# Performance work log

Hardware: AMD Instinct MI355X
Metric: run time of the kernel (lower is better)

Reference implementation:

```python
import jax, jax.numpy as jnp
import numpy as np

BSZ, T, D_IN, P, H, D_OUT = 8, 4096, 512, 256, 256, 512


def setup_inputs() -> dict:
    key = jax.random.key(0)
    ks = jax.random.split(key, 8)
    x_seq = jax.random.normal(ks[0], (BSZ, T, D_IN), dtype=jnp.float32)
    # stable diagonal transition: |a| < 1 so the 4096-step recurrence does not blow up
    a = jax.random.uniform(ks[1], (H,), minval=-0.99, maxval=0.99, dtype=jnp.float32)
    B = jax.random.normal(ks[2], (P, H), dtype=jnp.float32) * 0.05
    C = jax.random.normal(ks[3], (H, P), dtype=jnp.float32) * 0.05
    Wi = jax.random.normal(ks[4], (P, D_IN), dtype=jnp.float32) * 0.05
    bi = jax.random.normal(ks[5], (P,), dtype=jnp.float32) * 0.05
    Wo = jax.random.normal(ks[6], (D_OUT, P), dtype=jnp.float32) * 0.05
    bo = jax.random.normal(ks[7], (D_OUT,), dtype=jnp.float32) * 0.05
    return {"x_seq": x_seq, "a": a, "B": B, "C": C, "Wi": Wi, "bi": bi, "Wo": Wo, "bo": bo}


def reference(x_seq, a, B, C, Wi, bi, Wo, bo):
    # proj_in + relu (eqx.nn.Linear: y = W @ x + b), vmapped over batch and time
    x_proj = jax.nn.relu(jnp.einsum("btd,pd->btp", x_seq, Wi) + bi)  # [Bsz,T,P]
    # precompute driving input u_t = B^T x_t for every step
    u = jnp.einsum("btp,ph->bth", x_proj, B)  # [Bsz,T,H]
    u_t = jnp.swapaxes(u, 0, 1)  # [T,Bsz,H] (scan over time)

    def step(h, u_step):  # h: [Bsz,H]
        h = a * h + u_step
        return h, h

    h0 = jnp.zeros((x_seq.shape[0], a.shape[0]), dtype=x_seq.dtype)
    _, hs = jax.lax.scan(step, h0, u_t)  # hs: [T,Bsz,H]
    # y_t = C^T h_t, then proj_out
    y_seq = jnp.einsum("tbh,hp->btp", hs, C)  # [Bsz,T,P]
    y_out = jnp.einsum("btp,op->bto", y_seq, Wo) + bo  # [Bsz,T,D_out]
    return y_out
```

## Files before the change

kernel.cpp:

```cpp
#include <hip/hip_runtime.h>

#define BSZN 8
#define TT 4096
#define DIN 512
#define PP 256
#define HHH 256
#define DOUT 512
#define LCH 32
#define NCH (TT / LCH)
#define NBLK (BSZN * NCH)
#define XPS 264

typedef __attribute__((ext_vector_type(8))) short bf16x8;
typedef __attribute__((ext_vector_type(4))) float f32x4;

static __device__ __forceinline__ unsigned short f2bf(float x) {
  union { float f; unsigned u; } t{x};
  unsigned r = t.u + 0x7fffu + ((t.u >> 16) & 1u);
  return (unsigned short)(r >> 16);
}


__global__ __launch_bounds__(256) void prep_k(
    const float* __restrict__ Wi, const float* __restrict__ Wo,
    const float* __restrict__ Cm, const float* __restrict__ Bm,
    unsigned short* __restrict__ Wi_t, unsigned short* __restrict__ B_t,
    unsigned short* __restrict__ C_t, unsigned short* __restrict__ Wo_t) {
  const int b = blockIdx.x, tid = threadIdx.x;
  if (b < 128) {
    const int idx = b * 1024 + tid * 4;
    const int row = idx >> 9, d = idx & 511;
    const float4 v = *(const float4*)(Wi + idx);
    uint2 w;
    w.x = (unsigned)f2bf(v.x) | ((unsigned)f2bf(v.y) << 16);
    w.y = (unsigned)f2bf(v.z) | ((unsigned)f2bf(v.w) << 16);
    const int tile = d >> 5, kc = (d >> 3) & 3, s = (kc + (row >> 1)) & 3;
    *(uint2*)(Wi_t + tile * 8192 + row * 32 + s * 8 + (d & 7)) = w;
  } else if (b < 192) {
    const int f = (b - 128) * 256 + tid;
    const int p = f >> 6, h = (f & 63) * 4;
    const float4 v = *(const float4*)(Bm + (size_t)p * HHH + h);
    const float vv[4] = {v.x, v.y, v.z, v.w};
    const int tile = p >> 5, kc = (p >> 3) & 3;
#pragma unroll
    for (int j = 0; j < 4; ++j) {
      const int row = h + j, s = (kc + (row >> 1)) & 3;
      B_t[tile * 8192 + row * 32 + s * 8 + (p & 7)] = f2bf(vv[j]);
    }
  } else if (b < 256) {
    const int f = (b - 192) * 256 + tid;
    const int h = f >> 6, p = (f & 63) * 4;
    const float4 v = *(const float4*)(Cm + (size_t)h * PP + p);
    const float vv[4] = {v.x, v.y, v.z, v.w};
    const int tile = h >> 5, kc = (h >> 3) & 3;
#pragma unroll
    for (int j = 0; j < 4; ++j) {
      const int row = p + j, s = (kc + (row >> 1)) & 3;
      C_t[tile * 8192 + row * 32 + s * 8 + (h & 7)] = f2bf(vv[j]);
    }
  } else {
    const int idx = (b - 256) * 1024 + tid * 4;
    const int o = idx >> 8, p = idx & 255;
    const float4 v = *(const float4*)(Wo + idx);
    uint2 w;
    w.x = (unsigned)f2bf(v.x) | ((unsigned)f2bf(v.y) << 16);
    w.y = (unsigned)f2bf(v.z) | ((unsigned)f2bf(v.w) << 16);
    const int tile = p >> 5, kc = (p >> 3) & 3, s = (kc + (o >> 1)) & 3;
    *(uint2*)(Wo_t + tile * 16384 + o * 32 + s * 8 + (p & 7)) = w;
  }
}

__global__ __launch_bounds__(256, 4) void s4_scan(
    const float* __restrict__ x, const float* __restrict__ a,
    const unsigned short* __restrict__ Wi_t, const float* __restrict__ bi,
    const unsigned short* __restrict__ B_t, unsigned int* __restrict__ hs0_g,
    float* __restrict__ carry_g) {
  __shared__ alignas(16) char smem[16896];
  unsigned short* xs = (unsigned short*)smem;
  unsigned short* xp = (unsigned short*)smem;

  const int tid = threadIdx.x, wave = tid >> 6, lane = tid & 63;
  const int l15 = lane & 15, q = lane >> 4;
  const int bc = blockIdx.x;
  const size_t row0 = (size_t)bc * LCH;
  const int wc = wave * 64;

  int wrot[4];
#pragma unroll
  for (int ni = 0; ni < 4; ++ni) {
    const int r = wc + ni * 16 + l15;
    wrot[ni] = r * 64 + (((q + (r >> 1)) & 3) << 4);
  }
  int xpb[2];
#pragma unroll
  for (int mi = 0; mi < 2; ++mi) xpb[mi] = (mi * 16 + l15) * XPS + q * 8;

  f32x4 acc[2][4];
#pragma unroll
  for (int i = 0; i < 2; ++i)
#pragma unroll
    for (int j = 0; j < 4; ++j) acc[i][j] = f32x4{0.f, 0.f, 0.f, 0.f};

  for (int hh = 0; hh < 2; ++hh) {
    {
      float4 xv[8];
#pragma unroll
      for (int i = 0; i < 8; ++i) {
        const int f = i * 256 + tid;
        xv[i] = *(const float4*)(x + (row0 + (f >> 6)) * DIN + hh * 256 +
                                 (f & 63) * 4);
      }
#pragma unroll
      for (int i = 0; i < 8; ++i) {
        const int f = i * 256 + tid;
        uint2 w;
        w.x = (unsigned)f2bf(xv[i].x) | ((unsigned)f2bf(xv[i].y) << 16);
        w.y = (unsigned)f2bf(xv[i].z) | ((unsigned)f2bf(xv[i].w) << 16);
        *(uint2*)(xs + (f >> 6) * XPS + (f & 63) * 4) = w;
      }
    }
    __syncthreads();
    const char* WiB = (const char*)Wi_t + hh * 8 * 16384;
    for (int t = 0; t < 4; ++t) {
      bf16x8 af[2][2], bfv[4][2];
#pragma unroll
      for (int mi = 0; mi < 2; ++mi) {
        af[mi][0] = *(const bf16x8*)(xs + xpb[mi] + t * 64);
        af[mi][1] = *(const bf16x8*)(xs + xpb[mi] + t * 64 + 32);
      }
#pragma unroll
      for (int ni = 0; ni < 4; ++ni) {
        bfv[ni][0] = *(const bf16x8*)(WiB + (t * 2) * 16384 + wrot[ni]);
        bfv[ni][1] = *(const bf16x8*)(WiB + (t * 2 + 1) * 16384 + wrot[ni]);
      }
#pragma unroll
      for (int kk = 0; kk < 2; ++kk)
#pragma unroll
        for (int mi = 0; mi < 2; ++mi)
#pragma unroll
          for (int ni = 0; ni < 4; ++ni)
            acc[mi][ni] = __builtin_amdgcn_mfma_f32_16x16x32_bf16(
                af[mi][kk], bfv[ni][kk], acc[mi][ni], 0, 0, 0);
    }
    __syncthreads();
  }

#pragma unroll
  for (int ni = 0; ni < 4; ++ni) {
    const int col = wc + ni * 16 + l15;
    const float bb = bi[col];
#pragma unroll
    for (int mi = 0; mi < 2; ++mi)
#pragma unroll
      for (int reg = 0; reg < 4; ++reg) {
        const int row = mi * 16 + q * 4 + reg;
        xp[row * XPS + col] = f2bf(fmaxf(acc[mi][ni][reg] + bb, 0.f));
      }
  }
  __syncthreads();

#pragma unroll
  for (int i = 0; i < 2; ++i)
#pragma unroll
    for (int j = 0; j < 4; ++j) acc[i][j] = f32x4{0.f, 0.f, 0.f, 0.f};
  {
    const char* BB = (const char*)B_t;
    for (int t = 0; t < 4; ++t) {
      bf16x8 af[2][2], bfv[4][2];
#pragma unroll
      for (int mi = 0; mi < 2; ++mi) {
        af[mi][0] = *(const bf16x8*)(xp + xpb[mi] + t * 64);
        af[mi][1] = *(const bf16x8*)(xp + xpb[mi] + t * 64 + 32);
      }
#pragma unroll
      for (int ni = 0; ni < 4; ++ni) {
        bfv[ni][0] = *(const bf16x8*)(BB + (t * 2) * 16384 + wrot[ni]);
        bfv[ni][1] = *(const bf16x8*)(BB + (t * 2 + 1) * 16384 + wrot[ni]);
      }
#pragma unroll
      for (int kk = 0; kk < 2; ++kk)
#pragma unroll
        for (int mi = 0; mi < 2; ++mi)
#pragma unroll
          for (int ni = 0; ni < 4; ++ni)
            acc[mi][ni] = __builtin_amdgcn_mfma_f32_16x16x32_bf16(
                af[mi][kk], bfv[ni][kk], acc[mi][ni], 0, 0, 0);
    }
  }

  float aC[4], Wz[4];
#pragma unroll
  for (int ni = 0; ni < 4; ++ni) aC[ni] = a[wc + ni * 16 + l15];
#pragma unroll
  for (int ni = 0; ni < 4; ++ni) {
    const float A = aC[ni];
    const float A2 = A * A, A4 = A2 * A2, A8 = A4 * A4, A16 = A8 * A8;
    const float A4q = ((q & 1) ? A4 : 1.f) * ((q & 2) ? A8 : 1.f);
    float W = 0.f;
#pragma unroll
    for (int mi = 0; mi < 2; ++mi) {
      f32x4 v = acc[mi][ni];
      v.y = fmaf(A, v.x, v.y);
      v.z = fmaf(A, v.y, v.z);
      v.w = fmaf(A, v.z, v.w);
      const float E = v.w;
      const float E0 = __shfl(E, l15, 64);
      const float E1 = __shfl(E, l15 + 16, 64);
      const float E2 = __shfl(E, l15 + 32, 64);
      const float E3 = __shfl(E, l15 + 48, 64);
      const float s1 = E0, s2 = fmaf(A4, s1, E1), s3 = fmaf(A4, s2, E2);
      const float s4 = fmaf(A4, s3, E3);
      const float Sq = (q == 0) ? 0.f : (q == 1) ? s1 : (q == 2) ? s2 : s3;
      const float sin_ = fmaf(A4q, W, Sq);
      v.x = fmaf(A, sin_, v.x);
      v.y = fmaf(A2, sin_, v.y);
      v.z = fmaf(A2 * A, sin_, v.z);
      v.w = fmaf(A4, sin_, v.w);
      acc[mi][ni] = v;
      W = fmaf(A16, W, s4);
    }
    Wz[ni] = W;
  }
  if (q == 0) {
#pragma unroll
    for (int ni = 0; ni < 4; ++ni)
      carry_g[(size_t)bc * HHH + wc + ni * 16 + l15] = Wz[ni];
  }
#pragma unroll
  for (int ni = 0; ni < 4; ++ni)
#pragma unroll
    for (int mi = 0; mi < 2; ++mi) {
      const f32x4 v = acc[mi][ni];
      uint2 pk;
      pk.x = (unsigned)f2bf(v.x) | ((unsigned)f2bf(v.y) << 16);
      pk.y = (unsigned)f2bf(v.z) | ((unsigned)f2bf(v.w) << 16);
      const size_t e =
          (((size_t)bc * 4 + wave) * 8 + ni * 2 + mi) * 64 + lane;
      *(uint2*)(hs0_g + e * 2) = pk;
    }
}

__global__ __launch_bounds__(256) void s4_prefix(
    const float* __restrict__ a, const float* __restrict__ carry_g,
    float* __restrict__ P_g) {
  const int b = blockIdx.x, t = threadIdx.x;
  float A = a[t];
#pragma unroll
  for (int j = 0; j < 5; ++j) A *= A;
  const float* cg = carry_g + (size_t)b * NCH * HHH + t;
  float* pg = P_g + (size_t)b * NCH * HHH + t;
  float P = 0.f;
  for (int c0 = 0; c0 < NCH; c0 += 16) {
    float cv[16];
#pragma unroll
    for (int i = 0; i < 16; ++i) cv[i] = cg[(size_t)(c0 + i) * HHH];
#pragma unroll
    for (int i = 0; i < 16; ++i) {
      pg[(size_t)(c0 + i) * HHH] = P;
      P = fmaf(A, P, cv[i]);
    }
  }
}

__global__ __launch_bounds__(256, 4) void s4_out(
    const float* __restrict__ a, const unsigned int* __restrict__ hs0_g,
    const float* __restrict__ P_g, const unsigned short* __restrict__ C_t,
    const unsigned short* __restrict__ Wo_t, const float* __restrict__ bo,
    float* __restrict__ out) {
  __shared__ alignas(16) char smem[16896];
  unsigned short* hsL = (unsigned short*)smem;

  const int tid = threadIdx.x, wave = tid >> 6, lane = tid & 63;
  const int l15 = lane & 15, q = lane >> 4;
  const int bc = blockIdx.x;
  const size_t row0 = (size_t)bc * LCH;
  const int wc = wave * 64;

  int wrot[4];
#pragma unroll
  for (int ni = 0; ni < 4; ++ni) {
    const int r = wc + ni * 16 + l15;
    wrot[ni] = r * 64 + (((q + (r >> 1)) & 3) << 4);
  }
  int crot[2][4];
#pragma unroll
  for (int g = 0; g < 2; ++g)
#pragma unroll
    for (int ni = 0; ni < 4; ++ni) {
      const int r = wave * 128 + g * 64 + ni * 16 + l15;
      crot[g][ni] = r * 64 + (((q + (r >> 1)) & 3) << 4);
    }
  int xpb[2];
#pragma unroll
  for (int mi = 0; mi < 2; ++mi) xpb[mi] = (mi * 16 + l15) * XPS + q * 8;

  f32x4 acc[2][4];
#pragma unroll
  for (int ni = 0; ni < 4; ++ni)
#pragma unroll
    for (int mi = 0; mi < 2; ++mi) {
      const size_t e =
          (((size_t)bc * 4 + wave) * 8 + ni * 2 + mi) * 64 + lane;
      const uint2 pk = *(const uint2*)(hs0_g + e * 2);
      f32x4 v;
      v.x = __uint_as_float(pk.x << 16);
      v.y = __uint_as_float(pk.x & 0xffff0000u);
      v.z = __uint_as_float(pk.y << 16);
      v.w = __uint_as_float(pk.y & 0xffff0000u);
      acc[mi][ni] = v;
    }
#pragma unroll
  for (int ni = 0; ni < 4; ++ni) {
    const int col = wc + ni * 16 + l15;
    const float A = a[col];
    const float P = P_g[(size_t)bc * HHH + col];
    const float A2 = A * A, A4 = A2 * A2, A8 = A4 * A4, A16 = A8 * A8;
    const float A4q = ((q & 1) ? A4 : 1.f) * ((q & 2) ? A8 : 1.f);
    float fm = A4q * A * P;
#pragma unroll
    for (int mi = 0; mi < 2; ++mi) {
      f32x4 v = acc[mi][ni];
      v.x += fm;
      v.y = fmaf(A, fm, v.y);
      v.z = fmaf(A2, fm, v.z);
      v.w = fmaf(A2 * A, fm, v.w);
      acc[mi][ni] = v;
      fm *= A16;
    }
  }
#pragma unroll
  for (int ni = 0; ni < 4; ++ni) {
    const int col = wc + ni * 16 + l15;
#pragma unroll
    for (int mi = 0; mi < 2; ++mi)
#pragma unroll
      for (int reg = 0; reg < 4; ++reg)
        hsL[(mi * 16 + q * 4 + reg) * XPS + col] = f2bf(acc[mi][ni][reg]);
  }
  __syncthreads();

#pragma unroll
  for (int i = 0; i < 2; ++i)
#pragma unroll
    for (int j = 0; j < 4; ++j) acc[i][j] = f32x4{0.f, 0.f, 0.f, 0.f};
  {
    const char* CB = (const char*)C_t;
    for (int t = 0; t < 4; ++t) {
      bf16x8 af[2][2], bfv[4][2];
#pragma unroll
      for (int mi = 0; mi < 2; ++mi) {
        af[mi][0] = *(const bf16x8*)(hsL + xpb[mi] + t * 64);
        af[mi][1] = *(const bf16x8*)(hsL + xpb[mi] + t * 64 + 32);
      }
#pragma unroll
      for (int ni = 0; ni < 4; ++ni) {
        bfv[ni][0] = *(const bf16x8*)(CB + (t * 2) * 16384 + wrot[ni]);
        bfv[ni][1] = *(const bf16x8*)(CB + (t * 2 + 1) * 16384 + wrot[ni]);
      }
#pragma unroll
      for (int kk = 0; kk < 2; ++kk)
#pragma unroll
        for (int mi = 0; mi < 2; ++mi)
#pragma unroll
          for (int ni = 0; ni < 4; ++ni)
            acc[mi][ni] = __builtin_amdgcn_mfma_f32_16x16x32_bf16(
                af[mi][kk], bfv[ni][kk], acc[mi][ni], 0, 0, 0);
    }
  }
  __syncthreads();

#pragma unroll
  for (int ni = 0; ni < 4; ++ni) {
    const int col = wc + ni * 16 + l15;
#pragma unroll
    for (int mi = 0; mi < 2; ++mi)
#pragma unroll
      for (int reg = 0; reg < 4; ++reg)
        hsL[(mi * 16 + q * 4 + reg) * XPS + col] = f2bf(acc[mi][ni][reg]);
  }
  __syncthreads();

  const char* WoB = (const char*)Wo_t;
#pragma unroll
  for (int g = 0; g < 2; ++g) {
    f32x4 oacc[2][4];
#pragma unroll
    for (int i = 0; i < 2; ++i)
#pragma unroll
      for (int j = 0; j < 4; ++j) oacc[i][j] = f32x4{0.f, 0.f, 0.f, 0.f};
    for (int t = 0; t < 8; ++t) {
      bf16x8 af[2], bfv[4];
#pragma unroll
      for (int mi = 0; mi < 2; ++mi)
        af[mi] = *(const bf16x8*)(hsL + xpb[mi] + t * 32);
#pragma unroll
      for (int ni = 0; ni < 4; ++ni)
        bfv[ni] = *(const bf16x8*)(WoB + t * 32768 + crot[g][ni]);
#pragma unroll
      for (int mi = 0; mi < 2; ++mi)
#pragma unroll
        for (int ni = 0; ni < 4; ++ni)
          oacc[mi][ni] = __builtin_amdgcn_mfma_f32_16x16x32_bf16(
              af[mi], bfv[ni], oacc[mi][ni], 0, 0, 0);
    }
#pragma unroll
    for (int ni = 0; ni < 4; ++ni) {
      const int ocol = wave * 128 + g * 64 + ni * 16 + l15;
      const float bb = bo[ocol];
#pragma unroll
      for (int mi = 0; mi < 2; ++mi)
#pragma unroll
        for (int reg = 0; reg < 4; ++reg) {
          const int row = mi * 16 + q * 4 + reg;
          out[(row0 + row) * DOUT + ocol] = oacc[mi][ni][reg] + bb;
        }
    }
  }
}

extern "C" void kernel_launch(void* const* d_in, const int* in_sizes, int n_in,
                              void* d_out, int out_size, void* d_ws,
                              size_t ws_size, hipStream_t stream) {
  const float* x  = (const float*)d_in[0];
  const float* a  = (const float*)d_in[1];
  const float* Bm = (const float*)d_in[2];
  const float* Cm = (const float*)d_in[3];
  const float* Wi = (const float*)d_in[4];
  const float* bi = (const float*)d_in[5];
  const float* Wo = (const float*)d_in[6];
  const float* bo = (const float*)d_in[7];
  float* out = (float*)d_out;

  char* ws = (char*)d_ws;
  unsigned short* Wi_t = (unsigned short*)ws; ws += (size_t)PP * DIN * 2;
  unsigned short* B_t  = (unsigned short*)ws; ws += (size_t)HHH * PP * 2;
  unsigned short* C_t  = (unsigned short*)ws; ws += (size_t)HHH * PP * 2;
  unsigned short* Wo_t = (unsigned short*)ws; ws += (size_t)DOUT * PP * 2;
  float* carry_g = (float*)ws; ws += (size_t)NBLK * HHH * 4;
  float* P_g     = (float*)ws; ws += (size_t)NBLK * HHH * 4;
  unsigned int* hs0_g = (unsigned int*)ws;

  prep_k<<<384, 256, 0, stream>>>(Wi, Wo, Cm, Bm, Wi_t, B_t, C_t, Wo_t);
  s4_scan<<<NBLK, 256, 0, stream>>>(x, a, Wi_t, bi, B_t, hs0_g, carry_g);
  s4_prefix<<<BSZN, 256, 0, stream>>>(a, carry_g, P_g);
  s4_out<<<NBLK, 256, 0, stream>>>(a, hs0_g, P_g, C_t, Wo_t, bo, out);
}
```

Measured before the change: 164.2 us.

## Double-buffer weight fragments in registers and stagger K order per block

Each MFMA k-loop in the scan and output kernels now prefetches the next step's weight fragments into a register double buffer. The k-order is also rotated by block index so blocks read different weight tiles at the same time. The hs0 intermediate and the final output use nontemporal loads and stores, and launch bounds drop from 4 to 2 waves per SIMD so the extra live registers fit. The aim is to hide global and L2 weight-load latency and cut cache pollution from streaming data. The cost is higher register pressure and possibly lower occupancy.

```diff
diff --git a/kernel.cpp b/kernel.cpp
--- a/kernel.cpp
+++ b/kernel.cpp
@@ -70,7 +70,7 @@
   }
 }
 
-__global__ __launch_bounds__(256, 4) void s4_scan(
+__global__ __launch_bounds__(256, 2) void s4_scan(
     const float* __restrict__ x, const float* __restrict__ a,
     const unsigned short* __restrict__ Wi_t, const float* __restrict__ bi,
     const unsigned short* __restrict__ B_t, unsigned int* __restrict__ hs0_g,
@@ -84,6 +84,7 @@
   const int bc = blockIdx.x;
   const size_t row0 = (size_t)bc * LCH;
   const int wc = wave * 64;
+  const int tb = bc & 3;
 
   int wrot[4];
 #pragma unroll
@@ -121,17 +122,32 @@
     }
     __syncthreads();
     const char* WiB = (const char*)Wi_t + hh * 8 * 16384;
-    for (int t = 0; t < 4; ++t) {
-      bf16x8 af[2][2], bfv[4][2];
+    bf16x8 pf[2][4][2];
+    {
+#pragma unroll
+      for (int ni = 0; ni < 4; ++ni) {
+        pf[0][ni][0] = *(const bf16x8*)(WiB + (tb * 2) * 16384 + wrot[ni]);
+        pf[0][ni][1] = *(const bf16x8*)(WiB + (tb * 2 + 1) * 16384 + wrot[ni]);
+      }
+    }
+#pragma unroll
+    for (int tt = 0; tt < 4; ++tt) {
+      const int cur = tt & 1, nxt = cur ^ 1;
+      const int tr = (tt + tb) & 3;
+      if (tt < 3) {
+        const int tn = (tt + 1 + tb) & 3;
+#pragma unroll
+        for (int ni = 0; ni < 4; ++ni) {
+          pf[nxt][ni][0] = *(const bf16x8*)(WiB + (tn * 2) * 16384 + wrot[ni]);
+          pf[nxt][ni][1] =
+              *(const bf16x8*)(WiB + (tn * 2 + 1) * 16384 + wrot[ni]);
+        }
+      }
+      bf16x8 af[2][2];
 #pragma unroll
       for (int mi = 0; mi < 2; ++mi) {
-        af[mi][0] = *(const bf16x8*)(xs + xpb[mi] + t * 64);
-        af[mi][1] = *(const bf16x8*)(xs + xpb[mi] + t * 64 + 32);
-      }
-#pragma unroll
-      for (int ni = 0; ni < 4; ++ni) {
-        bfv[ni][0] = *(const bf16x8*)(WiB + (t * 2) * 16384 + wrot[ni]);
-        bfv[ni][1] = *(const bf16x8*)(WiB + (t * 2 + 1) * 16384 + wrot[ni]);
+        af[mi][0] = *(const bf16x8*)(xs + xpb[mi] + tr * 64);
+        af[mi][1] = *(const bf16x8*)(xs + xpb[mi] + tr * 64 + 32);
       }
 #pragma unroll
       for (int kk = 0; kk < 2; ++kk)
@@ -140,7 +156,7 @@
 #pragma unroll
           for (int ni = 0; ni < 4; ++ni)
             acc[mi][ni] = __builtin_amdgcn_mfma_f32_16x16x32_bf16(
-                af[mi][kk], bfv[ni][kk], acc[mi][ni], 0, 0, 0);
+                af[mi][kk], pf[cur][ni][kk], acc[mi][ni], 0, 0, 0);
     }
     __syncthreads();
   }
@@ -165,17 +181,30 @@
     for (int j = 0; j < 4; ++j) acc[i][j] = f32x4{0.f, 0.f, 0.f, 0.f};
   {
     const char* BB = (const char*)B_t;
-    for (int t = 0; t < 4; ++t) {
-      bf16x8 af[2][2], bfv[4][2];
+    bf16x8 pf[2][4][2];
+#pragma unroll
+    for (int ni = 0; ni < 4; ++ni) {
+      pf[0][ni][0] = *(const bf16x8*)(BB + (tb * 2) * 16384 + wrot[ni]);
+      pf[0][ni][1] = *(const bf16x8*)(BB + (tb * 2 + 1) * 16384 + wrot[ni]);
+    }
+#pragma unroll
+    for (int tt = 0; tt < 4; ++tt) {
+      const int cur = tt & 1, nxt = cur ^ 1;
+      const int tr = (tt + tb) & 3;
+      if (tt < 3) {
+        const int tn = (tt + 1 + tb) & 3;
+#pragma unroll
+        for (int ni = 0; ni < 4; ++ni) {
+          pf[nxt][ni][0] = *(const bf16x8*)(BB + (tn * 2) * 16384 + wrot[ni]);
+          pf[nxt][ni][1] =
+              *(const bf16x8*)(BB + (tn * 2 + 1) * 16384 + wrot[ni]);
+        }
+      }
+      bf16x8 af[2][2];
 #pragma unroll
       for (int mi = 0; mi < 2; ++mi) {
-        af[mi][0] = *(const bf16x8*)(xp + xpb[mi] + t * 64);
-        af[mi][1] = *(const bf16x8*)(xp + xpb[mi] + t * 64 + 32);
-      }
-#pragma unroll
-      for (int ni = 0; ni < 4; ++ni) {
-        bfv[ni][0] = *(const bf16x8*)(BB + (t * 2) * 16384 + wrot[ni]);
-        bfv[ni][1] = *(const bf16x8*)(BB + (t * 2 + 1) * 16384 + wrot[ni]);
+        af[mi][0] = *(const bf16x8*)(xp + xpb[mi] + tr * 64);
+        af[mi][1] = *(const bf16x8*)(xp + xpb[mi] + tr * 64 + 32);
       }
 #pragma unroll
       for (int kk = 0; kk < 2; ++kk)
@@ -184,7 +213,7 @@
 #pragma unroll
           for (int ni = 0; ni < 4; ++ni)
             acc[mi][ni] = __builtin_amdgcn_mfma_f32_16x16x32_bf16(
-                af[mi][kk], bfv[ni][kk], acc[mi][ni], 0, 0, 0);
+                af[mi][kk], pf[cur][ni][kk], acc[mi][ni], 0, 0, 0);
     }
   }
 
@@ -231,12 +260,16 @@
 #pragma unroll
     for (int mi = 0; mi < 2; ++mi) {
       const f32x4 v = acc[mi][ni];
-      uint2 pk;
-      pk.x = (unsigned)f2bf(v.x) | ((unsigned)f2bf(v.y) << 16);
-      pk.y = (unsigned)f2bf(v.z) | ((unsigned)f2bf(v.w) << 16);
+      unsigned long long pk =
+          (unsigned long long)((unsigned)f2bf(v.x) |
+                               ((unsigned)f2bf(v.y) << 16)) |
+          ((unsigned long long)((unsigned)f2bf(v.z) |
+                                ((unsigned)f2bf(v.w) << 16))
+           << 32);
       const size_t e =
           (((size_t)bc * 4 + wave) * 8 + ni * 2 + mi) * 64 + lane;
-      *(uint2*)(hs0_g + e * 2) = pk;
+      __builtin_nontemporal_store(
+          pk, (unsigned long long*)(hs0_g + e * 2));
     }
 }
 
@@ -262,7 +295,7 @@
   }
 }
 
-__global__ __launch_bounds__(256, 4) void s4_out(
+__global__ __launch_bounds__(256, 2) void s4_out(
     const float* __restrict__ a, const unsigned int* __restrict__ hs0_g,
     const float* __restrict__ P_g, const unsigned short* __restrict__ C_t,
     const unsigned short* __restrict__ Wo_t, const float* __restrict__ bo,
@@ -275,6 +308,7 @@
   const int bc = blockIdx.x;
   const size_t row0 = (size_t)bc * LCH;
   const int wc = wave * 64;
+  const int tb = bc & 3, tb8 = bc & 7;
 
   int wrot[4];
 #pragma unroll
@@ -301,12 +335,13 @@
     for (int mi = 0; mi < 2; ++mi) {
       const size_t e =
           (((size_t)bc * 4 + wave) * 8 + ni * 2 + mi) * 64 + lane;
-      const uint2 pk = *(const uint2*)(hs0_g + e * 2);
+      const unsigned long long pk = __builtin_nontemporal_load(
+          (const unsigned long long*)(hs0_g + e * 2));
       f32x4 v;
-      v.x = __uint_as_float(pk.x << 16);
-      v.y = __uint_as_float(pk.x & 0xffff0000u);
-      v.z = __uint_as_float(pk.y << 16);
-      v.w = __uint_as_float(pk.y & 0xffff0000u);
+      v.x = __uint_as_float((unsigned)(pk & 0xffffu) << 16);
+      v.y = __uint_as_float((unsigned)(pk & 0xffff0000u));
+      v.z = __uint_as_float((unsigned)((pk >> 32) & 0xffffu) << 16);
+      v.w = __uint_as_float((unsigned)((pk >> 48) & 0xffffu) << 16);
       acc[mi][ni] = v;
     }
 #pragma unroll
@@ -345,17 +380,30 @@
     for (int j = 0; j < 4; ++j) acc[i][j] = f32x4{0.f, 0.f, 0.f, 0.f};
   {
     const char* CB = (const char*)C_t;
-    for (int t = 0; t < 4; ++t) {
-      bf16x8 af[2][2], bfv[4][2];
+    bf16x8 pf[2][4][2];
+#pragma unroll
+    for (int ni = 0; ni < 4; ++ni) {
+      pf[0][ni][0] = *(const bf16x8*)(CB + (tb * 2) * 16384 + wrot[ni]);
+      pf[0][ni][1] = *(const bf16x8*)(CB + (tb * 2 + 1) * 16384 + wrot[ni]);
+    }
+#pragma unroll
+    for (int tt = 0; tt < 4; ++tt) {
+      const int cur = tt & 1, nxt = cur ^ 1;
+      const int tr = (tt + tb) & 3;
+      if (tt < 3) {
+        const int tn = (tt + 1 + tb) & 3;
+#pragma unroll
+        for (int ni = 0; ni < 4; ++ni) {
+          pf[nxt][ni][0] = *(const bf16x8*)(CB + (tn * 2) * 16384 + wrot[ni]);
+          pf[nxt][ni][1] =
+              *(const bf16x8*)(CB + (tn * 2 + 1) * 16384 + wrot[ni]);
+        }
+      }
+      bf16x8 af[2][2];
 #pragma unroll
       for (int mi = 0; mi < 2; ++mi) {
-        af[mi][0] = *(const bf16x8*)(hsL + xpb[mi] + t * 64);
-        af[mi][1] = *(const bf16x8*)(hsL + xpb[mi] + t * 64 + 32);
-      }
-#pragma unroll
-      for (int ni = 0; ni < 4; ++ni) {
-        bfv[ni][0] = *(const bf16x8*)(CB + (t * 2) * 16384 + wrot[ni]);
-        bfv[ni][1] = *(const bf16x8*)(CB + (t * 2 + 1) * 16384 + wrot[ni]);
+        af[mi][0] = *(const bf16x8*)(hsL + xpb[mi] + tr * 64);
+        af[mi][1] = *(const bf16x8*)(hsL + xpb[mi] + tr * 64 + 32);
       }
 #pragma unroll
       for (int kk = 0; kk < 2; ++kk)
@@ -364,7 +412,7 @@
 #pragma unroll
           for (int ni = 0; ni < 4; ++ni)
             acc[mi][ni] = __builtin_amdgcn_mfma_f32_16x16x32_bf16(
-                af[mi][kk], bfv[ni][kk], acc[mi][ni], 0, 0, 0);
+                af[mi][kk], pf[cur][ni][kk], acc[mi][ni], 0, 0, 0);
     }
   }
   __syncthreads();
@@ -388,20 +436,30 @@
     for (int i = 0; i < 2; ++i)
 #pragma unroll
       for (int j = 0; j < 4; ++j) oacc[i][j] = f32x4{0.f, 0.f, 0.f, 0.f};
-    for (int t = 0; t < 8; ++t) {
-      bf16x8 af[2], bfv[4];
+    bf16x8 pf[2][4];
+#pragma unroll
+    for (int ni = 0; ni < 4; ++ni)
+      pf[0][ni] = *(const bf16x8*)(WoB + tb8 * 32768 + crot[g][ni]);
+#pragma unroll
+    for (int tt = 0; tt < 8; ++tt) {
+      const int cur = tt & 1, nxt = cur ^ 1;
+      const int tr = (tt + tb8) & 7;
+      if (tt < 7) {
+        const int tn = (tt + 1 + tb8) & 7;
+#pragma unroll
+        for (int ni = 0; ni < 4; ++ni)
+          pf[nxt][ni] = *(const bf16x8*)(WoB + tn * 32768 + crot[g][ni]);
+      }
+      bf16x8 af[2];
 #pragma unroll
       for (int mi = 0; mi < 2; ++mi)
-        af[mi] = *(const bf16x8*)(hsL + xpb[mi] + t * 32);
-#pragma unroll
-      for (int ni = 0; ni < 4; ++ni)
-        bfv[ni] = *(const bf16x8*)(WoB + t * 32768 + crot[g][ni]);
+        af[mi] = *(const bf16x8*)(hsL + xpb[mi] + tr * 32);
 #pragma unroll
       for (int mi = 0; mi < 2; ++mi)
 #pragma unroll
         for (int ni = 0; ni < 4; ++ni)
           oacc[mi][ni] = __builtin_amdgcn_mfma_f32_16x16x32_bf16(
-              af[mi], bfv[ni], oacc[mi][ni], 0, 0, 0);
+              af[mi], pf[cur][ni], oacc[mi][ni], 0, 0, 0);
     }
 #pragma unroll
     for (int ni = 0; ni < 4; ++ni) {
@@ -412,7 +470,9 @@
 #pragma unroll
         for (int reg = 0; reg < 4; ++reg) {
           const int row = mi * 16 + q * 4 + reg;
-          out[(row0 + row) * DOUT + ocol] = oacc[mi][ni][reg] + bb;
+          __builtin_nontemporal_store(
+              oacc[mi][ni][reg] + bb,
+              &out[(row0 + row) * DOUT + ocol]);
         }
     }
   }
```

After: 164.6 us. Within noise of the previous version (+0.3%).
